# Optimization experiments

Hardware: AMD Instinct MI355X
Metric: run time of the kernel (lower is better)

The kernel has to match this reference:

```python
import jax, jax.numpy as jnp
import numpy as np

B, D, SLOTS, TOPK, CODE, ANCH = 8192, 64, 32, 3, 128, 32
BETA = 0.25  # vq_commitment_beta


def _clinear(zr, zi, Wr, Wi, br, bi):
    # ComplexLinear: real = Wr(zr)-Wi(zi), imag = Wi(zr)+Wr(zi); each nn.Linear carries its own bias
    return (zr @ Wr + br) - (zi @ Wi + bi), (zr @ Wi + bi) + (zi @ Wr + br)


def _layernorm(x, g, b, eps=1e-6):
    m = x.mean(-1, keepdims=True)
    v = ((x - m) ** 2).mean(-1, keepdims=True)  # biased var, as torch LayerNorm
    return (x - m) / jnp.sqrt(v + eps) * g + b


def setup_inputs() -> dict:
    key = jax.random.key(0)
    ks = jax.random.split(key, 16)
    f = jax.random.normal
    s = 0.05
    rng_init = 1.0 / np.sqrt(D)
    return dict(
        curr_r=f(ks[0], (B, D)), curr_i=f(ks[1], (B, D)),
        mem_r=f(ks[2], (B, SLOTS, D)), mem_i=f(ks[3], (B, SLOTS, D)),
        codebook=jax.random.uniform(ks[4], (CODE, 2 * D), minval=-rng_init, maxval=rng_init),
        qkv_Wr=f(ks[5], (3, D, D)) * s, qkv_Wi=f(ks[6], (3, D, D)) * s,
        qkv_br=jnp.zeros((3, D)), qkv_bi=jnp.zeros((3, D)),
        quad_Wr=f(ks[7], (D, D)) * s, quad_Wi=f(ks[8], (D, D)) * s,
        quad_br=jnp.zeros((D,)), quad_bi=jnp.zeros((D,)),
        sens_Wr=f(ks[9], (D, D)) * s, sens_Wi=f(ks[10], (D, D)) * s,
        sens_br=jnp.zeros((D,)), sens_bi=jnp.zeros((D,)),
        vis_palette=f(ks[11], (ANCH, 2 * D)), aud_palette=f(ks[12], (ANCH, 2 * D)),
        gate_W=f(ks[13], (2 * D, 1)) * s, gate_b=jnp.zeros((1,)),
        addr_W=f(ks[14], (2 * D, SLOTS)) * s, addr_b=jnp.zeros((SLOTS,)),
        ln_gamma_r=jnp.ones((D,)), ln_beta_r=jnp.zeros((D,)),
        ln_gamma_i=jnp.ones((D,)), ln_beta_i=jnp.zeros((D,)),
    )


def reference(curr_r, curr_i, mem_r, mem_i, codebook,
              qkv_Wr, qkv_Wi, qkv_br, qkv_bi,
              quad_Wr, quad_Wi, quad_br, quad_bi,
              sens_Wr, sens_Wi, sens_br, sens_bi,
              vis_palette, aud_palette,
              gate_W, gate_b, addr_W, addr_b,
              ln_gamma_r, ln_beta_r, ln_gamma_i, ln_beta_i):
    sg = jax.lax.stop_gradient
    z_flat = jnp.concatenate([curr_r, curr_i], -1)  # [B,2D]

    # ---- EMA_VQ (eval path): argmin codebook lookup + straight-through ----
    d = (z_flat ** 2).sum(1, keepdims=True) + (codebook ** 2).sum(1) - 2.0 * z_flat @ codebook.T
    d = jnp.maximum(d, 0.0)
    indices = jnp.argmin(d, -1)                      # [B]
    z_q = codebook[indices]                          # [B,2D]
    vq_loss = BETA * ((sg(z_q) - z_flat) ** 2).mean(-1)
    z_q = z_flat + sg(z_q - z_flat)
    probs = jnp.zeros((CODE,), z_flat.dtype).at[indices].add(1.0) / B
    norm_entropy = -(probs * jnp.log(probs + 1e-10)).sum() / np.log(CODE)
    vq_r, vq_i = z_q[..., :D], z_q[..., D:]

    # ---- HermitianGating ----
    qr, qi = _clinear(curr_r, curr_i, qkv_Wr[0], qkv_Wi[0], qkv_br[0], qkv_bi[0])
    kr, ki = _clinear(curr_r, curr_i, qkv_Wr[1], qkv_Wi[1], qkv_br[1], qkv_bi[1])
    vr, vi = _clinear(curr_r, curr_i, qkv_Wr[2], qkv_Wi[2], qkv_br[2], qkv_bi[2])
    gate = jax.nn.sigmoid((qr * kr + qi * ki).sum(-1, keepdims=True))
    g_r, g_i = vr * gate, vi * gate

    # ---- AssociativeMemory: softmax read + topk scatter write ----
    sim = jnp.einsum('bsd,bd->bs', mem_r, curr_r) + jnp.einsum('bsd,bd->bs', mem_i, curr_i)
    sim = sim - sg(sim.max(-1, keepdims=True))
    attn = jax.nn.softmax(sim, -1)
    read_r = jnp.einsum('bs,bsd->bd', attn, mem_r)
    read_i = jnp.einsum('bs,bsd->bd', attn, mem_i)
    write_gate = jax.nn.sigmoid(z_flat @ gate_W + gate_b)[:, :, None]  # [B,1,1]
    logits = z_flat @ addr_W + addr_b
    logits = logits - sg(logits.max(-1, keepdims=True))
    ww = jax.nn.softmax(logits, -1)                  # [B,SLOTS]
    slot_entropy = (-(ww * jnp.log(ww + 1e-10)).sum(-1)).mean()
    top_vals, top_idx = jax.lax.top_k(ww, TOPK)
    sparse = jnp.zeros_like(ww).at[jnp.arange(B)[:, None], top_idx].set(top_vals)
    sparse = sparse / (sparse.sum(-1, keepdims=True) + 1e-6)
    eff = write_gate * sparse[..., None]             # [B,SLOTS,1]
    nm_r = jnp.tanh(mem_r + eff * (curr_r[:, None, :] - mem_r))
    nm_i = jnp.tanh(mem_i + eff * (curr_i[:, None, :] - mem_i))
    nm_r = _layernorm(nm_r, ln_gamma_r, ln_beta_r)
    nm_i = _layernorm(nm_i, ln_gamma_i, ln_beta_i)

    # ---- SubmodalityAnchorModule ----
    s_r, s_i = _clinear(curr_r, curr_i, sens_Wr, sens_Wi, sens_br, sens_bi)
    sflat = jnp.concatenate([s_r, s_i], -1)

    def attend(pal):
        sc = sflat @ pal.T
        sc = sc - sg(sc.max(-1, keepdims=True))
        return jax.nn.softmax(sc, -1) @ pal

    vis = attend(vis_palette)
    aud = attend(aud_palette)
    exp_r = vis[..., :D] - aud[..., D:]   # vis_c + i*aud_c
    exp_i = vis[..., D:] + aud[..., :D]

    # ---- QuadratureModule: multiply by i ----
    zr, zi = _clinear(curr_r, curr_i, quad_Wr, quad_Wi, quad_br, quad_bi)
    q_r, q_i = -zi, zr

    combined = jnp.concatenate(
        [vq_r, vq_i, g_r, g_i, read_r, read_i, exp_r, exp_i, q_r, q_i,
         nm_r.reshape(B, -1), nm_i.reshape(B, -1)], -1)  # [B, 10*D + 2*SLOTS*D]
    return combined, vq_loss, indices, slot_entropy, norm_entropy
```

## Files before the change

### kernel.cpp

```cpp
#include <hip/hip_runtime.h>
#include <hip/hip_bf16.h>


#define NROWS 8
#define NBLOCKS 1024
#define RSTRIDE 4736

static constexpr size_t OFF_VQLOSS = 38797312UL;
static constexpr size_t OFF_IDX    = 38805504UL;
static constexpr size_t OFF_SENT   = 38813696UL;
static constexpr size_t OFF_NENT   = 38813697UL;

struct Params {
  const float* curr_r; const float* curr_i;
  const float* mem_r;  const float* mem_i;
  const float* codebook;
  const float* qkv_Wr; const float* qkv_Wi; const float* qkv_br; const float* qkv_bi;
  const float* quad_Wr; const float* quad_Wi; const float* quad_br; const float* quad_bi;
  const float* sens_Wr; const float* sens_Wi; const float* sens_br; const float* sens_bi;
  const float* vis_pal; const float* aud_pal;
  const float* gate_W; const float* gate_b;
  const float* addr_W; const float* addr_b;
  const float* ln_gr; const float* ln_br; const float* ln_gi; const float* ln_bi;
  float* out;
  int* hist;
  float* rowent;
};

__global__ __launch_bounds__(256) void row_main(Params P) {
  const int b = blockIdx.x;
  const int t = threadIdx.x;
  const int lane = t & 63;
  const int wv = t >> 6;

  __shared__ float zr[64], zi[64];
  __shared__ float s_qr[64], s_qi[64], s_kr[64], s_ki[64], s_vr[64], s_vi[64];
  __shared__ float sfl[128];
  __shared__ float s_sp[4][4][64];
  __shared__ float lp[4][32];
  __shared__ float s_eff[32];
  __shared__ float s_sim[32], s_attn[32];
  __shared__ float s_rr[4][8][8], s_ri[4][8][8];
  __shared__ float s_pv[4][32], s_pa[4][32];
  __shared__ float s_pvp[32], s_pap[32];
  __shared__ float s_vo[128], s_ao[128];
  __shared__ float s_wg, s_gate;

  const size_t bb = (size_t)b;
  const int s = t >> 3, k = t & 7, d0 = k * 8;
  const float* mrp = P.mem_r + ((bb * 32 + s) * 64 + d0);
  const float* mip = P.mem_i + ((bb * 32 + s) * 64 + d0);
  float4 a0 = *(const float4*)mrp, a1 = *(const float4*)(mrp + 4);
  float4 b0 = *(const float4*)mip, b1 = *(const float4*)(mip + 4);
  float mr[8] = {a0.x, a0.y, a0.z, a0.w, a1.x, a1.y, a1.z, a1.w};
  float mi[8] = {b0.x, b0.y, b0.z, b0.w, b1.x, b1.y, b1.z, b1.w};

  if (t < 64)       zr[t]      = P.curr_r[bb * 64 + t];
  else if (t < 128) zi[t - 64] = P.curr_i[bb * 64 + (t - 64)];
  __syncthreads();

  float* orow = P.out + bb * RSTRIDE;

  {
    const int j = lane, cl = wv;
    const float *Wr, *Wi, *br_, *bi_;
    if      (cl == 0) { Wr = P.qkv_Wr;        Wi = P.qkv_Wi;        br_ = P.qkv_br;       bi_ = P.qkv_bi;       }
    else if (cl == 1) { Wr = P.qkv_Wr + 4096; Wi = P.qkv_Wi + 4096; br_ = P.qkv_br + 64;  bi_ = P.qkv_bi + 64;  }
    else if (cl == 2) { Wr = P.qkv_Wr + 8192; Wi = P.qkv_Wi + 8192; br_ = P.qkv_br + 128; bi_ = P.qkv_bi + 128; }
    else              { Wr = P.quad_Wr;       Wi = P.quad_Wi;       br_ = P.quad_br;      bi_ = P.quad_bi;      }
    float aRR = 0.f, aRI = 0.f, aIR = 0.f, aII = 0.f;
    for (int d = 0; d < 64; ++d) {
      const float xr = zr[d], xi = zi[d];
      const float wr = Wr[d * 64 + j], wi = Wi[d * 64 + j];
      aRR += xr * wr; aRI += xr * wi; aIR += xi * wr; aII += xi * wi;
    }
    const float oR = (aRR + br_[j]) - (aII + bi_[j]);
    const float oI = (aRI + bi_[j]) + (aIR + br_[j]);
    if      (cl == 0) { s_qr[j] = oR; s_qi[j] = oI; }
    else if (cl == 1) { s_kr[j] = oR; s_ki[j] = oI; }
    else if (cl == 2) { s_vr[j] = oR; s_vi[j] = oI; }
    else              { orow[512 + j] = -oI; orow[576 + j] = oR; }
    float bRR = 0.f, bRI = 0.f, bIR = 0.f, bII = 0.f;
    for (int dd = 0; dd < 16; ++dd) {
      const int d = wv * 16 + dd;
      const float xr = zr[d], xi = zi[d];
      const float wr = P.sens_Wr[d * 64 + j], wi = P.sens_Wi[d * 64 + j];
      bRR += xr * wr; bRI += xr * wi; bIR += xi * wr; bII += xi * wi;
    }
    s_sp[wv][0][j] = bRR; s_sp[wv][1][j] = bRI; s_sp[wv][2][j] = bIR; s_sp[wv][3][j] = bII;
  }
  __syncthreads();

  {
    float sp = 0.f;
    #pragma unroll
    for (int x = 0; x < 8; ++x) sp += mr[x] * zr[d0 + x] + mi[x] * zi[d0 + x];
    sp += __shfl_xor(sp, 1); sp += __shfl_xor(sp, 2); sp += __shfl_xor(sp, 4);
    if (k == 0) s_sim[s] = sp;
  }
  if (t < 128) {
    const int q = t >> 5, l = t & 31;
    const float* zz = (q < 2) ? zr : zi;
    const int zb = (q & 1) * 32;
    float a = 0.f;
    for (int i = 0; i < 32; ++i) a += zz[zb + i] * P.addr_W[(q * 32 + i) * 32 + l];
    lp[q][l] = a;
  } else if (t < 192) {
    const int j = t - 128;
    float tw = zr[j] * P.gate_W[j] + zi[j] * P.gate_W[64 + j];
    #pragma unroll
    for (int m = 1; m <= 32; m <<= 1) tw += __shfl_xor(tw, m);
    if (j == 0) s_wg = tw;
  } else {
    const int j = t - 192;
    float g = s_qr[j] * s_kr[j] + s_qi[j] * s_ki[j];
    #pragma unroll
    for (int m = 1; m <= 32; m <<= 1) g += __shfl_xor(g, m);
    if (j == 0) s_gate = 1.f / (1.f + expf(-g));
  }
  __syncthreads();

  if (t < 32) {
    float v = s_sim[t];
    float mx = v;
    #pragma unroll
    for (int m = 16; m >= 1; m >>= 1) mx = fmaxf(mx, __shfl_xor(mx, m));
    float e = expf(v - mx);
    float sm = e;
    #pragma unroll
    for (int m = 16; m >= 1; m >>= 1) sm += __shfl_xor(sm, m);
    s_attn[t] = e / sm;
  } else if (t >= 64 && t < 96) {
    const int l = t - 64;
    float lg = lp[0][l] + lp[1][l] + lp[2][l] + lp[3][l] + P.addr_b[l];
    float mx = lg;
    #pragma unroll
    for (int m = 16; m >= 1; m >>= 1) mx = fmaxf(mx, __shfl_xor(mx, m));
    float e = expf(lg - mx);
    float sm = e;
    #pragma unroll
    for (int m = 16; m >= 1; m >>= 1) sm += __shfl_xor(sm, m);
    const float w = e / sm;
    float es = -(w * logf(w + 1e-10f));
    #pragma unroll
    for (int m = 16; m >= 1; m >>= 1) es += __shfl_xor(es, m);
    if (l == 0) P.rowent[b] = es;
    const float myw = w;
    bool picked = false;
    float val = w; int idx = l;
    float sumtop = 0.f;
    #pragma unroll
    for (int it = 0; it < 3; ++it) {
      float v2 = val; int i2 = idx;
      #pragma unroll
      for (int m = 16; m >= 1; m >>= 1) {
        float ov = __shfl_xor(v2, m); int oi = __shfl_xor(i2, m);
        if (ov > v2 || (ov == v2 && oi < i2)) { v2 = ov; i2 = oi; }
      }
      sumtop += v2;
      if (l == i2) { picked = true; val = -1e30f; }
    }
    const float wgate = 1.f / (1.f + expf(-(s_wg + P.gate_b[0])));
    s_eff[l] = picked ? wgate * (myw / (sumtop + 1e-6f)) : 0.f;
  } else if (t >= 128 && t < 192) {
    const int j = t - 128;
    const float aRR = s_sp[0][0][j] + s_sp[1][0][j] + s_sp[2][0][j] + s_sp[3][0][j];
    const float aRI = s_sp[0][1][j] + s_sp[1][1][j] + s_sp[2][1][j] + s_sp[3][1][j];
    const float aIR = s_sp[0][2][j] + s_sp[1][2][j] + s_sp[2][2][j] + s_sp[3][2][j];
    const float aII = s_sp[0][3][j] + s_sp[1][3][j] + s_sp[2][3][j] + s_sp[3][3][j];
    const float oR = (aRR + P.sens_br[j]) - (aII + P.sens_bi[j]);
    const float oI = (aRI + P.sens_bi[j]) + (aIR + P.sens_br[j]);
    sfl[j] = oR; sfl[64 + j] = oI;
  }
  __syncthreads();

  const float aw = s_attn[s];
  {
    float pr[8], pi[8];
    #pragma unroll
    for (int x = 0; x < 8; ++x) { pr[x] = aw * mr[x]; pi[x] = aw * mi[x]; }
    #pragma unroll
    for (int m = 8; m <= 32; m <<= 1) {
      #pragma unroll
      for (int x = 0; x < 8; ++x) { pr[x] += __shfl_xor(pr[x], m); pi[x] += __shfl_xor(pi[x], m); }
    }
    if (lane < 8) {
      #pragma unroll
      for (int x = 0; x < 8; ++x) { s_rr[wv][lane][x] = pr[x]; s_ri[wv][lane][x] = pi[x]; }
    }
  }
  {
    const float eff = s_eff[s];
    float nr[8], ni[8];
    #pragma unroll
    for (int x = 0; x < 8; ++x) {
      nr[x] = tanhf(mr[x] + eff * (zr[d0 + x] - mr[x]));
      ni[x] = tanhf(mi[x] + eff * (zi[d0 + x] - mi[x]));
    }
    float sR = 0.f, sI = 0.f;
    #pragma unroll
    for (int x = 0; x < 8; ++x) { sR += nr[x]; sI += ni[x]; }
    sR += __shfl_xor(sR, 1); sR += __shfl_xor(sR, 2); sR += __shfl_xor(sR, 4);
    sI += __shfl_xor(sI, 1); sI += __shfl_xor(sI, 2); sI += __shfl_xor(sI, 4);
    const float mR = sR * (1.f / 64.f), mI = sI * (1.f / 64.f);
    float vR = 0.f, vI = 0.f;
    #pragma unroll
    for (int x = 0; x < 8; ++x) {
      float dr = nr[x] - mR; vR += dr * dr;
      float di = ni[x] - mI; vI += di * di;
    }
    vR += __shfl_xor(vR, 1); vR += __shfl_xor(vR, 2); vR += __shfl_xor(vR, 4);
    vI += __shfl_xor(vI, 1); vI += __shfl_xor(vI, 2); vI += __shfl_xor(vI, 4);
    const float invR = 1.f / sqrtf(vR * (1.f / 64.f) + 1e-6f);
    const float invI = 1.f / sqrtf(vI * (1.f / 64.f) + 1e-6f);
    float oR[8], oI[8];
    #pragma unroll
    for (int x = 0; x < 8; ++x) {
      const int d = d0 + x;
      oR[x] = (nr[x] - mR) * invR * P.ln_gr[d] + P.ln_br[d];
      oI[x] = (ni[x] - mI) * invI * P.ln_gi[d] + P.ln_bi[d];
    }
    *(float4*)&orow[640 + s * 64 + d0]      = make_float4(oR[0], oR[1], oR[2], oR[3]);
    *(float4*)&orow[640 + s * 64 + d0 + 4]  = make_float4(oR[4], oR[5], oR[6], oR[7]);
    *(float4*)&orow[2688 + s * 64 + d0]     = make_float4(oI[0], oI[1], oI[2], oI[3]);
    *(float4*)&orow[2688 + s * 64 + d0 + 4] = make_float4(oI[4], oI[5], oI[6], oI[7]);
  }
  if (t < 128) {
    const int a = t & 31, q = t >> 5;
    float sc = 0.f;
    for (int x = q * 32; x < q * 32 + 32; ++x) sc += sfl[x] * P.vis_pal[a * 128 + x];
    s_pv[q][a] = sc;
  } else {
    const int tt = t - 128, a = tt & 31, q = tt >> 5;
    float sc = 0.f;
    for (int x = q * 32; x < q * 32 + 32; ++x) sc += sfl[x] * P.aud_pal[a * 128 + x];
    s_pa[q][a] = sc;
  }
  __syncthreads();

  if (t < 64) {
    const int kk = t >> 3, xx = t & 7;
    float rv = s_rr[0][kk][xx] + s_rr[1][kk][xx] + s_rr[2][kk][xx] + s_rr[3][kk][xx];
    float iv = s_ri[0][kk][xx] + s_ri[1][kk][xx] + s_ri[2][kk][xx] + s_ri[3][kk][xx];
    orow[256 + t] = rv;
    orow[320 + t] = iv;
  } else if (t >= 128 && t < 160) {
    const int a = t - 128;
    float sc = s_pv[0][a] + s_pv[1][a] + s_pv[2][a] + s_pv[3][a];
    float mx = sc;
    #pragma unroll
    for (int m = 16; m >= 1; m >>= 1) mx = fmaxf(mx, __shfl_xor(mx, m));
    float e = expf(sc - mx);
    float sm = e;
    #pragma unroll
    for (int m = 16; m >= 1; m >>= 1) sm += __shfl_xor(sm, m);
    s_pvp[a] = e / sm;
  } else if (t >= 192 && t < 224) {
    const int a = t - 192;
    float sc = s_pa[0][a] + s_pa[1][a] + s_pa[2][a] + s_pa[3][a];
    float mx = sc;
    #pragma unroll
    for (int m = 16; m >= 1; m >>= 1) mx = fmaxf(mx, __shfl_xor(mx, m));
    float e = expf(sc - mx);
    float sm = e;
    #pragma unroll
    for (int m = 16; m >= 1; m >>= 1) sm += __shfl_xor(sm, m);
    s_pap[a] = e / sm;
  }
  __syncthreads();

  if (t < 128) {
    float v = 0.f;
    for (int a = 0; a < 32; ++a) v += s_pvp[a] * P.vis_pal[a * 128 + t];
    s_vo[t] = v;
  } else {
    const int j = t - 128;
    float v = 0.f;
    for (int a = 0; a < 32; ++a) v += s_pap[a] * P.aud_pal[a * 128 + j];
    s_ao[j] = v;
  }
  if (t < 64)       orow[128 + t] = s_vr[t] * s_gate;
  else if (t < 128) orow[192 + (t - 64)] = s_vi[t - 64] * s_gate;
  __syncthreads();

  if (t < 64)       orow[384 + t] = s_vo[t] - s_ao[64 + t];
  else if (t < 128) orow[448 + (t - 64)] = s_vo[t] + s_ao[t - 64];
}

__global__ __launch_bounds__(256) void vq_kernel(Params P) {
  const int t = threadIdx.x;
  const int bid = blockIdx.x;
  const int lane = t & 63;
  const int wv = t >> 6;

  __shared__ __align__(16) float s_zr[NROWS][64], s_zi[NROWS][64];
  __shared__ double s_cbn[128];
  __shared__ double s_dall[NROWS][256];
  __shared__ float s_vqls[NROWS];
  __shared__ int s_idx[NROWS];

  {
    const float* cr = P.curr_r + (size_t)bid * (NROWS * 64);
    const float* ci = P.curr_i + (size_t)bid * (NROWS * 64);
    float* zr = &s_zr[0][0];
    float* zi = &s_zi[0][0];
    for (int i = t; i < NROWS * 64; i += 256) { zr[i] = cr[i]; zi[i] = ci[i]; }
  }
  {
    const float* cb = P.codebook + (t & 127) * 128 + (t >> 7) * 64;
    double a = 0.0;
    for (int d = 0; d < 64; ++d) { double w = (double)cb[d]; a = fma(w, w, a); }
    s_dall[0][t] = a;
    __syncthreads();
    if (t < 128) s_cbn[t] = s_dall[0][t] + s_dall[0][t + 128];
    __syncthreads();
  }
  {
    const int c = t & 127, h = t >> 7;
    const float* cb = P.codebook + c * 128 + h * 64;
    const float (*zb)[64] = h ? s_zi : s_zr;
    double acc[NROWS];
    #pragma unroll
    for (int r = 0; r < NROWS; ++r) acc[r] = 0.0;
    for (int d = 0; d < 64; ++d) {
      const double w = (double)cb[d];
      #pragma unroll
      for (int r = 0; r < NROWS; ++r) acc[r] = fma(w, (double)zb[r][d], acc[r]);
    }
    #pragma unroll
    for (int r = 0; r < NROWS; ++r) s_dall[r][h * 128 + c] = acc[r];
    __syncthreads();
    #pragma unroll
    for (int rr = 0; rr < 2; ++rr) {
      const int r = wv * 2 + rr;
      const double d0 = s_cbn[lane]      - 2.0 * (s_dall[r][lane]      + s_dall[r][128 + lane]);
      const double d1 = s_cbn[lane + 64] - 2.0 * (s_dall[r][64 + lane] + s_dall[r][192 + lane]);
      double sv = d0; int si = lane;
      if (d1 < sv) { sv = d1; si = lane + 64; }
      #pragma unroll
      for (int m = 1; m <= 32; m <<= 1) {
        double ov = __shfl_xor(sv, m);
        int oi = __shfl_xor(si, m);
        if (ov < sv || (ov == sv && oi < si)) { sv = ov; si = oi; }
      }
      if (lane == 0) { s_idx[r] = si; atomicAdd(&P.hist[si], 1); }
    }
    __syncthreads();
  }
  {
    #pragma unroll
    for (int rr = 0; rr < 2; ++rr) {
      const int r = wv * 2 + rr;
      const float* cb = P.codebook + (size_t)s_idx[r] * 128;
      float d0_ = cb[lane] - s_zr[r][lane];
      float d1_ = cb[64 + lane] - s_zi[r][lane];
      float v = d0_ * d0_ + d1_ * d1_;
      #pragma unroll
      for (int m = 1; m <= 32; m <<= 1) v += __shfl_xor(v, m);
      if (lane == 0) s_vqls[r] = 0.25f * v * (1.0f / 128.0f);
    }
  }
  __syncthreads();
  {
    const int j = t & 63, g = t >> 6;
    #pragma unroll
    for (int rr = 0; rr < 4; ++rr) {
      const int r = (g >> 1) * 4 + rr;
      float* orow = P.out + ((size_t)bid * NROWS + r) * RSTRIDE;
      const float* cb = P.codebook + (size_t)s_idx[r] * 128;
      if ((g & 1) == 0) {
        float z = s_zr[r][j];
        orow[j] = z + (cb[j] - z);
      } else {
        float z = s_zi[r][j];
        orow[64 + j] = z + (cb[64 + j] - z);
      }
    }
  }
  if (t < NROWS) {
    P.out[OFF_VQLOSS + (size_t)bid * NROWS + t] = s_vqls[t];
    P.out[OFF_IDX + (size_t)bid * NROWS + t] = (float)s_idx[t];
  }
}

__global__ __launch_bounds__(256) void finalize_k(const int* hist, const float* rowent,
                                                  float* out) {
  const int t = threadIdx.x;
  __shared__ float red[256];
  float se = 0.f;
  for (int i = t; i < 8192; i += 256) se += rowent[i];
  red[t] = se;
  __syncthreads();
  for (int off = 128; off >= 1; off >>= 1) {
    if (t < off) red[t] += red[t + off];
    __syncthreads();
  }
  if (t == 0) out[OFF_SENT] = red[0] / 8192.0f;
  __syncthreads();
  float ne = 0.f;
  if (t < 128) {
    const float pp = (float)hist[t] / 8192.0f;
    ne = -(pp * logf(pp + 1e-10f));
  }
  red[t] = ne;
  __syncthreads();
  for (int off = 128; off >= 1; off >>= 1) {
    if (t < off) red[t] += red[t + off];
    __syncthreads();
  }
  if (t == 0) out[OFF_NENT] = red[0] / logf(128.0f);
}

extern "C" void kernel_launch(void* const* d_in, const int* in_sizes, int n_in,
                              void* d_out, int out_size, void* d_ws, size_t ws_size,
                              hipStream_t stream) {
  (void)in_sizes; (void)n_in; (void)out_size; (void)ws_size;
  Params P;
  P.curr_r   = (const float*)d_in[0];
  P.curr_i   = (const float*)d_in[1];
  P.mem_r    = (const float*)d_in[2];
  P.mem_i    = (const float*)d_in[3];
  P.codebook = (const float*)d_in[4];
  P.qkv_Wr   = (const float*)d_in[5];
  P.qkv_Wi   = (const float*)d_in[6];
  P.qkv_br   = (const float*)d_in[7];
  P.qkv_bi   = (const float*)d_in[8];
  P.quad_Wr  = (const float*)d_in[9];
  P.quad_Wi  = (const float*)d_in[10];
  P.quad_br  = (const float*)d_in[11];
  P.quad_bi  = (const float*)d_in[12];
  P.sens_Wr  = (const float*)d_in[13];
  P.sens_Wi  = (const float*)d_in[14];
  P.sens_br  = (const float*)d_in[15];
  P.sens_bi  = (const float*)d_in[16];
  P.vis_pal  = (const float*)d_in[17];
  P.aud_pal  = (const float*)d_in[18];
  P.gate_W   = (const float*)d_in[19];
  P.gate_b   = (const float*)d_in[20];
  P.addr_W   = (const float*)d_in[21];
  P.addr_b   = (const float*)d_in[22];
  P.ln_gr    = (const float*)d_in[23];
  P.ln_br    = (const float*)d_in[24];
  P.ln_gi    = (const float*)d_in[25];
  P.ln_bi    = (const float*)d_in[26];
  P.out = (float*)d_out;
  P.hist = (int*)d_ws;
  P.rowent = (float*)((char*)d_ws + 512);

  hipMemsetAsync(d_ws, 0, 512, stream);
  row_main<<<dim3(8192), dim3(256), 0, stream>>>(P);
  vq_kernel<<<dim3(NBLOCKS), dim3(256), 0, stream>>>(P);
  finalize_k<<<dim3(1), dim3(256), 0, stream>>>(P.hist, P.rowent, (float*)d_out);
}
```

Baseline: 252.3 us.

## Restructure per-row kernel into wave-specialized stages with fewer block barriers

```diff
diff --git a/kernel.cpp b/kernel.cpp
--- a/kernel.cpp
+++ b/kernel.cpp
@@ -27,264 +27,247 @@
   float* rowent;
 };
 
-__global__ __launch_bounds__(256) void row_main(Params P) {
+__global__ __launch_bounds__(256) void row_wave(Params P) {
   const int b = blockIdx.x;
   const int t = threadIdx.x;
   const int lane = t & 63;
   const int wv = t >> 6;
 
   __shared__ float zr[64], zi[64];
-  __shared__ float s_qr[64], s_qi[64], s_kr[64], s_ki[64], s_vr[64], s_vi[64];
   __shared__ float sfl[128];
-  __shared__ float s_sp[4][4][64];
-  __shared__ float lp[4][32];
   __shared__ float s_eff[32];
-  __shared__ float s_sim[32], s_attn[32];
-  __shared__ float s_rr[4][8][8], s_ri[4][8][8];
-  __shared__ float s_pv[4][32], s_pa[4][32];
+  __shared__ float s_vr[64], s_vi[64];
+  __shared__ float s_vo[128], s_ao[128];
   __shared__ float s_pvp[32], s_pap[32];
-  __shared__ float s_vo[128], s_ao[128];
-  __shared__ float s_wg, s_gate;
+  __shared__ float s_attn[32];
+  __shared__ float s_gate_s;
 
   const size_t bb = (size_t)b;
-  const int s = t >> 3, k = t & 7, d0 = k * 8;
-  const float* mrp = P.mem_r + ((bb * 32 + s) * 64 + d0);
-  const float* mip = P.mem_i + ((bb * 32 + s) * 64 + d0);
-  float4 a0 = *(const float4*)mrp, a1 = *(const float4*)(mrp + 4);
-  float4 b0 = *(const float4*)mip, b1 = *(const float4*)(mip + 4);
-  float mr[8] = {a0.x, a0.y, a0.z, a0.w, a1.x, a1.y, a1.z, a1.w};
-  float mi[8] = {b0.x, b0.y, b0.z, b0.w, b1.x, b1.y, b1.z, b1.w};
+  const size_t mbase = bb * 2048;
+  float* orow = P.out + bb * RSTRIDE;
 
   if (t < 64)       zr[t]      = P.curr_r[bb * 64 + t];
   else if (t < 128) zi[t - 64] = P.curr_i[bb * 64 + (t - 64)];
   __syncthreads();
 
-  float* orow = P.out + bb * RSTRIDE;
-
-  {
-    const int j = lane, cl = wv;
-    const float *Wr, *Wi, *br_, *bi_;
-    if      (cl == 0) { Wr = P.qkv_Wr;        Wi = P.qkv_Wi;        br_ = P.qkv_br;       bi_ = P.qkv_bi;       }
-    else if (cl == 1) { Wr = P.qkv_Wr + 4096; Wi = P.qkv_Wi + 4096; br_ = P.qkv_br + 64;  bi_ = P.qkv_bi + 64;  }
-    else if (cl == 2) { Wr = P.qkv_Wr + 8192; Wi = P.qkv_Wi + 8192; br_ = P.qkv_br + 128; bi_ = P.qkv_bi + 128; }
-    else              { Wr = P.quad_Wr;       Wi = P.quad_Wi;       br_ = P.quad_br;      bi_ = P.quad_bi;      }
+  if (wv == 0) {
+    const int j = lane;
     float aRR = 0.f, aRI = 0.f, aIR = 0.f, aII = 0.f;
     for (int d = 0; d < 64; ++d) {
       const float xr = zr[d], xi = zi[d];
-      const float wr = Wr[d * 64 + j], wi = Wi[d * 64 + j];
+      const float wr = P.sens_Wr[d * 64 + j], wi = P.sens_Wi[d * 64 + j];
       aRR += xr * wr; aRI += xr * wi; aIR += xi * wr; aII += xi * wi;
     }
-    const float oR = (aRR + br_[j]) - (aII + bi_[j]);
-    const float oI = (aRI + bi_[j]) + (aIR + br_[j]);
-    if      (cl == 0) { s_qr[j] = oR; s_qi[j] = oI; }
-    else if (cl == 1) { s_kr[j] = oR; s_ki[j] = oI; }
-    else if (cl == 2) { s_vr[j] = oR; s_vi[j] = oI; }
-    else              { orow[512 + j] = -oI; orow[576 + j] = oR; }
-    float bRR = 0.f, bRI = 0.f, bIR = 0.f, bII = 0.f;
-    for (int dd = 0; dd < 16; ++dd) {
-      const int d = wv * 16 + dd;
-      const float xr = zr[d], xi = zi[d];
-      const float wr = P.sens_Wr[d * 64 + j], wi = P.sens_Wi[d * 64 + j];
-      bRR += xr * wr; bRI += xr * wi; bIR += xi * wr; bII += xi * wi;
-    }
-    s_sp[wv][0][j] = bRR; s_sp[wv][1][j] = bRI; s_sp[wv][2][j] = bIR; s_sp[wv][3][j] = bII;
-  }
-  __syncthreads();
-
-  {
-    float sp = 0.f;
-    #pragma unroll
-    for (int x = 0; x < 8; ++x) sp += mr[x] * zr[d0 + x] + mi[x] * zi[d0 + x];
-    sp += __shfl_xor(sp, 1); sp += __shfl_xor(sp, 2); sp += __shfl_xor(sp, 4);
-    if (k == 0) s_sim[s] = sp;
-  }
-  if (t < 128) {
-    const int q = t >> 5, l = t & 31;
-    const float* zz = (q < 2) ? zr : zi;
-    const int zb = (q & 1) * 32;
-    float a = 0.f;
-    for (int i = 0; i < 32; ++i) a += zz[zb + i] * P.addr_W[(q * 32 + i) * 32 + l];
-    lp[q][l] = a;
-  } else if (t < 192) {
-    const int j = t - 128;
-    float tw = zr[j] * P.gate_W[j] + zi[j] * P.gate_W[64 + j];
+    sfl[j]      = (aRR + P.sens_br[j]) - (aII + P.sens_bi[j]);
+    sfl[64 + j] = (aRI + P.sens_bi[j]) + (aIR + P.sens_br[j]);
+  } else if (wv == 1) {
+    float tw = zr[lane] * P.gate_W[lane] + zi[lane] * P.gate_W[64 + lane];
     #pragma unroll
     for (int m = 1; m <= 32; m <<= 1) tw += __shfl_xor(tw, m);
-    if (j == 0) s_wg = tw;
+    const float wgate = 1.f / (1.f + expf(-(tw + P.gate_b[0])));
+    if (lane < 32) {
+      const int l = lane;
+      float lg = P.addr_b[l];
+      for (int d = 0; d < 64; ++d) lg += zr[d] * P.addr_W[d * 32 + l];
+      for (int d = 0; d < 64; ++d) lg += zi[d] * P.addr_W[(64 + d) * 32 + l];
+      float mx = lg;
+      #pragma unroll
+      for (int m = 16; m >= 1; m >>= 1) mx = fmaxf(mx, __shfl_xor(mx, m));
+      float e = expf(lg - mx);
+      float sm = e;
+      #pragma unroll
+      for (int m = 16; m >= 1; m >>= 1) sm += __shfl_xor(sm, m);
+      const float w = e / sm;
+      float es = -(w * logf(w + 1e-10f));
+      #pragma unroll
+      for (int m = 16; m >= 1; m >>= 1) es += __shfl_xor(es, m);
+      if (l == 0) P.rowent[b] = es;
+      const float myw = w;
+      bool picked = false;
+      float val = w; int idx = l;
+      float sumtop = 0.f;
+      #pragma unroll
+      for (int it = 0; it < 3; ++it) {
+        float v2 = val; int i2 = idx;
+        #pragma unroll
+        for (int m = 16; m >= 1; m >>= 1) {
+          float ov = __shfl_xor(v2, m); int oi = __shfl_xor(i2, m);
+          if (ov > v2 || (ov == v2 && oi < i2)) { v2 = ov; i2 = oi; }
+        }
+        sumtop += v2;
+        if (l == i2) { picked = true; val = -1e30f; }
+      }
+      s_eff[l] = picked ? wgate * (myw / (sumtop + 1e-6f)) : 0.f;
+    }
+  } else if (wv == 2) {
+    const int j = lane;
+    float qR, qI, kR, kI;
+    {
+      float aRR = 0.f, aRI = 0.f, aIR = 0.f, aII = 0.f;
+      for (int d = 0; d < 64; ++d) {
+        const float xr = zr[d], xi = zi[d];
+        const float wr = P.qkv_Wr[d * 64 + j], wi = P.qkv_Wi[d * 64 + j];
+        aRR += xr * wr; aRI += xr * wi; aIR += xi * wr; aII += xi * wi;
+      }
+      qR = (aRR + P.qkv_br[j]) - (aII + P.qkv_bi[j]);
+      qI = (aRI + P.qkv_bi[j]) + (aIR + P.qkv_br[j]);
+    }
+    {
+      float aRR = 0.f, aRI = 0.f, aIR = 0.f, aII = 0.f;
+      for (int d = 0; d < 64; ++d) {
+        const float xr = zr[d], xi = zi[d];
+        const float wr = P.qkv_Wr[4096 + d * 64 + j], wi = P.qkv_Wi[4096 + d * 64 + j];
+        aRR += xr * wr; aRI += xr * wi; aIR += xi * wr; aII += xi * wi;
+      }
+      kR = (aRR + P.qkv_br[64 + j]) - (aII + P.qkv_bi[64 + j]);
+      kI = (aRI + P.qkv_bi[64 + j]) + (aIR + P.qkv_br[64 + j]);
+    }
+    float g = qR * kR + qI * kI;
+    #pragma unroll
+    for (int m = 1; m <= 32; m <<= 1) g += __shfl_xor(g, m);
+    if (lane == 0) s_gate_s = 1.f / (1.f + expf(-g));
   } else {
-    const int j = t - 192;
-    float g = s_qr[j] * s_kr[j] + s_qi[j] * s_ki[j];
-    #pragma unroll
-    for (int m = 1; m <= 32; m <<= 1) g += __shfl_xor(g, m);
-    if (j == 0) s_gate = 1.f / (1.f + expf(-g));
-  }
-  __syncthreads();
-
-  if (t < 32) {
-    float v = s_sim[t];
-    float mx = v;
-    #pragma unroll
-    for (int m = 16; m >= 1; m >>= 1) mx = fmaxf(mx, __shfl_xor(mx, m));
-    float e = expf(v - mx);
-    float sm = e;
-    #pragma unroll
-    for (int m = 16; m >= 1; m >>= 1) sm += __shfl_xor(sm, m);
-    s_attn[t] = e / sm;
-  } else if (t >= 64 && t < 96) {
-    const int l = t - 64;
-    float lg = lp[0][l] + lp[1][l] + lp[2][l] + lp[3][l] + P.addr_b[l];
-    float mx = lg;
-    #pragma unroll
-    for (int m = 16; m >= 1; m >>= 1) mx = fmaxf(mx, __shfl_xor(mx, m));
-    float e = expf(lg - mx);
-    float sm = e;
-    #pragma unroll
-    for (int m = 16; m >= 1; m >>= 1) sm += __shfl_xor(sm, m);
-    const float w = e / sm;
-    float es = -(w * logf(w + 1e-10f));
-    #pragma unroll
-    for (int m = 16; m >= 1; m >>= 1) es += __shfl_xor(es, m);
-    if (l == 0) P.rowent[b] = es;
-    const float myw = w;
-    bool picked = false;
-    float val = w; int idx = l;
-    float sumtop = 0.f;
-    #pragma unroll
-    for (int it = 0; it < 3; ++it) {
-      float v2 = val; int i2 = idx;
-      #pragma unroll
-      for (int m = 16; m >= 1; m >>= 1) {
-        float ov = __shfl_xor(v2, m); int oi = __shfl_xor(i2, m);
-        if (ov > v2 || (ov == v2 && oi < i2)) { v2 = ov; i2 = oi; }
-      }
-      sumtop += v2;
-      if (l == i2) { picked = true; val = -1e30f; }
-    }
-    const float wgate = 1.f / (1.f + expf(-(s_wg + P.gate_b[0])));
-    s_eff[l] = picked ? wgate * (myw / (sumtop + 1e-6f)) : 0.f;
-  } else if (t >= 128 && t < 192) {
-    const int j = t - 128;
-    const float aRR = s_sp[0][0][j] + s_sp[1][0][j] + s_sp[2][0][j] + s_sp[3][0][j];
-    const float aRI = s_sp[0][1][j] + s_sp[1][1][j] + s_sp[2][1][j] + s_sp[3][1][j];
-    const float aIR = s_sp[0][2][j] + s_sp[1][2][j] + s_sp[2][2][j] + s_sp[3][2][j];
-    const float aII = s_sp[0][3][j] + s_sp[1][3][j] + s_sp[2][3][j] + s_sp[3][3][j];
-    const float oR = (aRR + P.sens_br[j]) - (aII + P.sens_bi[j]);
-    const float oI = (aRI + P.sens_bi[j]) + (aIR + P.sens_br[j]);
-    sfl[j] = oR; sfl[64 + j] = oI;
-  }
-  __syncthreads();
-
-  const float aw = s_attn[s];
-  {
-    float pr[8], pi[8];
-    #pragma unroll
-    for (int x = 0; x < 8; ++x) { pr[x] = aw * mr[x]; pi[x] = aw * mi[x]; }
-    #pragma unroll
-    for (int m = 8; m <= 32; m <<= 1) {
-      #pragma unroll
-      for (int x = 0; x < 8; ++x) { pr[x] += __shfl_xor(pr[x], m); pi[x] += __shfl_xor(pi[x], m); }
-    }
-    if (lane < 8) {
-      #pragma unroll
-      for (int x = 0; x < 8; ++x) { s_rr[wv][lane][x] = pr[x]; s_ri[wv][lane][x] = pi[x]; }
-    }
-  }
-  {
-    const float eff = s_eff[s];
-    float nr[8], ni[8];
-    #pragma unroll
-    for (int x = 0; x < 8; ++x) {
-      nr[x] = tanhf(mr[x] + eff * (zr[d0 + x] - mr[x]));
-      ni[x] = tanhf(mi[x] + eff * (zi[d0 + x] - mi[x]));
-    }
-    float sR = 0.f, sI = 0.f;
-    #pragma unroll
-    for (int x = 0; x < 8; ++x) { sR += nr[x]; sI += ni[x]; }
-    sR += __shfl_xor(sR, 1); sR += __shfl_xor(sR, 2); sR += __shfl_xor(sR, 4);
-    sI += __shfl_xor(sI, 1); sI += __shfl_xor(sI, 2); sI += __shfl_xor(sI, 4);
+    const int j = lane;
+    {
+      float aRR = 0.f, aRI = 0.f, aIR = 0.f, aII = 0.f;
+      for (int d = 0; d < 64; ++d) {
+        const float xr = zr[d], xi = zi[d];
+        const float wr = P.qkv_Wr[8192 + d * 64 + j], wi = P.qkv_Wi[8192 + d * 64 + j];
+        aRR += xr * wr; aRI += xr * wi; aIR += xi * wr; aII += xi * wi;
+      }
+      s_vr[j] = (aRR + P.qkv_br[128 + j]) - (aII + P.qkv_bi[128 + j]);
+      s_vi[j] = (aRI + P.qkv_bi[128 + j]) + (aIR + P.qkv_br[128 + j]);
+    }
+    {
+      float aRR = 0.f, aRI = 0.f, aIR = 0.f, aII = 0.f;
+      for (int d = 0; d < 64; ++d) {
+        const float xr = zr[d], xi = zi[d];
+        const float wr = P.quad_Wr[d * 64 + j], wi = P.quad_Wi[d * 64 + j];
+        aRR += xr * wr; aRI += xr * wi; aIR += xi * wr; aII += xi * wi;
+      }
+      const float oR = (aRR + P.quad_br[j]) - (aII + P.quad_bi[j]);
+      const float oI = (aRI + P.quad_bi[j]) + (aIR + P.quad_br[j]);
+      orow[512 + j] = -oI;
+      orow[576 + j] = oR;
+    }
+  }
+  __syncthreads();
+
+  const float gR_ = P.ln_gr[lane], bR_ = P.ln_br[lane];
+  const float gI_ = P.ln_gi[lane], bI_ = P.ln_bi[lane];
+
+  auto do_nm = [&](int s2) {
+    const float a = P.mem_r[mbase + s2 * 64 + lane];
+    const float c = P.mem_i[mbase + s2 * 64 + lane];
+    const float e = s_eff[s2];
+    const float nr = tanhf(a + e * (zr[lane] - a));
+    const float ni = tanhf(c + e * (zi[lane] - c));
+    float sR = nr, sI = ni;
+    #pragma unroll
+    for (int m = 1; m <= 32; m <<= 1) { sR += __shfl_xor(sR, m); sI += __shfl_xor(sI, m); }
     const float mR = sR * (1.f / 64.f), mI = sI * (1.f / 64.f);
-    float vR = 0.f, vI = 0.f;
-    #pragma unroll
-    for (int x = 0; x < 8; ++x) {
-      float dr = nr[x] - mR; vR += dr * dr;
-      float di = ni[x] - mI; vI += di * di;
-    }
-    vR += __shfl_xor(vR, 1); vR += __shfl_xor(vR, 2); vR += __shfl_xor(vR, 4);
-    vI += __shfl_xor(vI, 1); vI += __shfl_xor(vI, 2); vI += __shfl_xor(vI, 4);
+    const float dr = nr - mR, di = ni - mI;
+    float vR = dr * dr, vI = di * di;
+    #pragma unroll
+    for (int m = 1; m <= 32; m <<= 1) { vR += __shfl_xor(vR, m); vI += __shfl_xor(vI, m); }
     const float invR = 1.f / sqrtf(vR * (1.f / 64.f) + 1e-6f);
     const float invI = 1.f / sqrtf(vI * (1.f / 64.f) + 1e-6f);
-    float oR[8], oI[8];
-    #pragma unroll
-    for (int x = 0; x < 8; ++x) {
-      const int d = d0 + x;
-      oR[x] = (nr[x] - mR) * invR * P.ln_gr[d] + P.ln_br[d];
-      oI[x] = (ni[x] - mI) * invI * P.ln_gi[d] + P.ln_bi[d];
-    }
-    *(float4*)&orow[640 + s * 64 + d0]      = make_float4(oR[0], oR[1], oR[2], oR[3]);
-    *(float4*)&orow[640 + s * 64 + d0 + 4]  = make_float4(oR[4], oR[5], oR[6], oR[7]);
-    *(float4*)&orow[2688 + s * 64 + d0]     = make_float4(oI[0], oI[1], oI[2], oI[3]);
-    *(float4*)&orow[2688 + s * 64 + d0 + 4] = make_float4(oI[4], oI[5], oI[6], oI[7]);
-  }
-  if (t < 128) {
-    const int a = t & 31, q = t >> 5;
-    float sc = 0.f;
-    for (int x = q * 32; x < q * 32 + 32; ++x) sc += sfl[x] * P.vis_pal[a * 128 + x];
-    s_pv[q][a] = sc;
+    orow[640  + s2 * 64 + lane] = dr * invR * gR_ + bR_;
+    orow[2688 + s2 * 64 + lane] = di * invI * gI_ + bI_;
+  };
+
+  if (wv == 0) {
+    if (lane < 32) {
+      float sc = 0.f;
+      const float* p = P.vis_pal + (size_t)lane * 128;
+      for (int x = 0; x < 128; ++x) sc += sfl[x] * p[x];
+      float mx = sc;
+      #pragma unroll
+      for (int m = 16; m >= 1; m >>= 1) mx = fmaxf(mx, __shfl_xor(mx, m));
+      float e = expf(sc - mx);
+      float sm = e;
+      #pragma unroll
+      for (int m = 16; m >= 1; m >>= 1) sm += __shfl_xor(sm, m);
+      s_pvp[lane] = e / sm;
+    }
+    float v0 = 0.f, v1 = 0.f;
+    for (int a = 0; a < 32; ++a) {
+      const float pw = s_pvp[a];
+      v0 += pw * P.vis_pal[a * 128 + lane];
+      v1 += pw * P.vis_pal[a * 128 + 64 + lane];
+    }
+    s_vo[lane] = v0; s_vo[64 + lane] = v1;
+    #pragma unroll
+    for (int s2 = 24; s2 < 28; ++s2) do_nm(s2);
+  } else if (wv == 1) {
+    if (lane < 32) {
+      float sc = 0.f;
+      const float* p = P.aud_pal + (size_t)lane * 128;
+      for (int x = 0; x < 128; ++x) sc += sfl[x] * p[x];
+      float mx = sc;
+      #pragma unroll
+      for (int m = 16; m >= 1; m >>= 1) mx = fmaxf(mx, __shfl_xor(mx, m));
+      float e = expf(sc - mx);
+      float sm = e;
+      #pragma unroll
+      for (int m = 16; m >= 1; m >>= 1) sm += __shfl_xor(sm, m);
+      s_pap[lane] = e / sm;
+    }
+    float v0 = 0.f, v1 = 0.f;
+    for (int a = 0; a < 32; ++a) {
+      const float pw = s_pap[a];
+      v0 += pw * P.aud_pal[a * 128 + lane];
+      v1 += pw * P.aud_pal[a * 128 + 64 + lane];
+    }
+    s_ao[lane] = v0; s_ao[64 + lane] = v1;
+    #pragma unroll
+    for (int s2 = 28; s2 < 32; ++s2) do_nm(s2);
+  } else if (wv == 2) {
+    const int s2 = lane >> 1, dh = (lane & 1) * 32;
+    float sp = 0.f;
+    {
+      const float* mrp = P.mem_r + mbase + s2 * 64 + dh;
+      const float* mip = P.mem_i + mbase + s2 * 64 + dh;
+      #pragma unroll
+      for (int c4 = 0; c4 < 32; c4 += 4) {
+        const float4 m4 = *(const float4*)&mrp[c4];
+        const float4 n4 = *(const float4*)&mip[c4];
+        sp += m4.x * zr[dh + c4]     + m4.y * zr[dh + c4 + 1]
+            + m4.z * zr[dh + c4 + 2] + m4.w * zr[dh + c4 + 3]
+            + n4.x * zi[dh + c4]     + n4.y * zi[dh + c4 + 1]
+            + n4.z * zi[dh + c4 + 2] + n4.w * zi[dh + c4 + 3];
+      }
+    }
+    sp += __shfl_xor(sp, 1);
+    float mx = sp;
+    #pragma unroll
+    for (int m = 1; m <= 32; m <<= 1) mx = fmaxf(mx, __shfl_xor(mx, m));
+    float e = expf(sp - mx);
+    float sm = e;
+    #pragma unroll
+    for (int m = 1; m <= 32; m <<= 1) sm += __shfl_xor(sm, m);
+    const float aw = e / (sm * 0.5f);
+    if ((lane & 1) == 0) s_attn[s2] = aw;
+    float rr = 0.f, ri = 0.f;
+    for (int s3 = 0; s3 < 32; ++s3) {
+      const float at = s_attn[s3];
+      rr += at * P.mem_r[mbase + s3 * 64 + lane];
+      ri += at * P.mem_i[mbase + s3 * 64 + lane];
+    }
+    orow[256 + lane] = rr;
+    orow[320 + lane] = ri;
+    #pragma unroll
+    for (int s3 = 16; s3 < 24; ++s3) do_nm(s3);
   } else {
-    const int tt = t - 128, a = tt & 31, q = tt >> 5;
-    float sc = 0.f;
-    for (int x = q * 32; x < q * 32 + 32; ++x) sc += sfl[x] * P.aud_pal[a * 128 + x];
-    s_pa[q][a] = sc;
-  }
-  __syncthreads();
-
-  if (t < 64) {
-    const int kk = t >> 3, xx = t & 7;
-    float rv = s_rr[0][kk][xx] + s_rr[1][kk][xx] + s_rr[2][kk][xx] + s_rr[3][kk][xx];
-    float iv = s_ri[0][kk][xx] + s_ri[1][kk][xx] + s_ri[2][kk][xx] + s_ri[3][kk][xx];
-    orow[256 + t] = rv;
-    orow[320 + t] = iv;
-  } else if (t >= 128 && t < 160) {
-    const int a = t - 128;
-    float sc = s_pv[0][a] + s_pv[1][a] + s_pv[2][a] + s_pv[3][a];
-    float mx = sc;
-    #pragma unroll
-    for (int m = 16; m >= 1; m >>= 1) mx = fmaxf(mx, __shfl_xor(mx, m));
-    float e = expf(sc - mx);
-    float sm = e;
-    #pragma unroll
-    for (int m = 16; m >= 1; m >>= 1) sm += __shfl_xor(sm, m);
-    s_pvp[a] = e / sm;
-  } else if (t >= 192 && t < 224) {
-    const int a = t - 192;
-    float sc = s_pa[0][a] + s_pa[1][a] + s_pa[2][a] + s_pa[3][a];
-    float mx = sc;
-    #pragma unroll
-    for (int m = 16; m >= 1; m >>= 1) mx = fmaxf(mx, __shfl_xor(mx, m));
-    float e = expf(sc - mx);
-    float sm = e;
-    #pragma unroll
-    for (int m = 16; m >= 1; m >>= 1) sm += __shfl_xor(sm, m);
-    s_pap[a] = e / sm;
-  }
-  __syncthreads();
-
-  if (t < 128) {
-    float v = 0.f;
-    for (int a = 0; a < 32; ++a) v += s_pvp[a] * P.vis_pal[a * 128 + t];
-    s_vo[t] = v;
-  } else {
-    const int j = t - 128;
-    float v = 0.f;
-    for (int a = 0; a < 32; ++a) v += s_pap[a] * P.aud_pal[a * 128 + j];
-    s_ao[j] = v;
-  }
-  if (t < 64)       orow[128 + t] = s_vr[t] * s_gate;
-  else if (t < 128) orow[192 + (t - 64)] = s_vi[t - 64] * s_gate;
-  __syncthreads();
-
-  if (t < 64)       orow[384 + t] = s_vo[t] - s_ao[64 + t];
-  else if (t < 128) orow[448 + (t - 64)] = s_vo[t] + s_ao[t - 64];
+    #pragma unroll
+    for (int s2 = 0; s2 < 16; ++s2) do_nm(s2);
+  }
+  __syncthreads();
+
+  if (wv == 0)      orow[128 + lane] = s_vr[lane] * s_gate_s;
+  else if (wv == 1) orow[192 + lane] = s_vi[lane] * s_gate_s;
+  else if (wv == 2) orow[384 + lane] = s_vo[lane] - s_ao[64 + lane];
+  else              orow[448 + lane] = s_vo[64 + lane] + s_ao[lane];
 }
 
 __global__ __launch_bounds__(256) void vq_kernel(Params P) {
@@ -448,7 +431,7 @@
   P.rowent = (float*)((char*)d_ws + 512);
 
   hipMemsetAsync(d_ws, 0, 512, stream);
-  row_main<<<dim3(8192), dim3(256), 0, stream>>>(P);
+  row_wave<<<dim3(8192), dim3(256), 0, stream>>>(P);
   vq_kernel<<<dim3(NBLOCKS), dim3(256), 0, stream>>>(P);
   finalize_k<<<dim3(1), dim3(256), 0, stream>>>(P.hist, P.rowent, (float*)d_out);
 }
```

Result: slower. 314.1 us (+24.5%).
